# Performance work log

Measured on AMD Instinct MI355X. Metric: run time of the kernel, lower is better.

## Reference

```python
import jax, jax.numpy as jnp
import numpy as np

B, N, F_IN, H = 1, 4096, 256, 4
OUT_F = 256
HEAD_DIM = OUT_F // H
E_RAND = 131072  # avg degree 32
LN_EPS = 1e-5


def setup_inputs() -> dict:
    key = jax.random.key(0)
    ks = jax.random.split(key, 12)
    x = jax.random.normal(ks[0], (B, N, F_IN), jnp.float32)
    # random edges + self-loops so every softmax row has at least one unmasked entry
    src = jax.random.randint(ks[1], (E_RAND,), 0, N, dtype=jnp.int32)
    dst = jax.random.randint(ks[2], (E_RAND,), 0, N, dtype=jnp.int32)
    loops = jnp.arange(N, dtype=jnp.int32)
    edge_index = jnp.stack([jnp.concatenate([loops, src]), jnp.concatenate([loops, dst])])
    s = 1.0 / np.sqrt(F_IN)
    Wq = jax.random.uniform(ks[3], (OUT_F, F_IN), jnp.float32, -s, s)
    bq = jax.random.uniform(ks[4], (OUT_F,), jnp.float32, -s, s)
    Wk = jax.random.uniform(ks[5], (OUT_F, F_IN), jnp.float32, -s, s)
    bk = jax.random.uniform(ks[6], (OUT_F,), jnp.float32, -s, s)
    Wv = jax.random.uniform(ks[7], (OUT_F, F_IN), jnp.float32, -s, s)
    bv = jax.random.uniform(ks[8], (OUT_F,), jnp.float32, -s, s)
    ln_g = jnp.ones((OUT_F,), jnp.float32)
    ln_b = jnp.zeros((OUT_F,), jnp.float32)
    return {"x": x, "edge_index": edge_index, "Wq": Wq, "bq": bq, "Wk": Wk,
            "bk": bk, "Wv": Wv, "bv": bv, "ln_g": ln_g, "ln_b": ln_b}


def _layer_norm(y, g, b):
    mu = jnp.mean(y, axis=-1, keepdims=True)
    var = jnp.mean(jnp.square(y - mu), axis=-1, keepdims=True)
    return (y - mu) * jax.lax.rsqrt(var + LN_EPS) * g + b


def reference(x, edge_index, Wq, bq, Wk, bk, Wv, bv, ln_g, ln_b):
    b, n, f_in = x.shape
    out_f = Wq.shape[0]
    hd = out_f // H
    # linear projections -> [b, H, n, hd]
    Q = (x @ Wq.T + bq).reshape(b, n, H, hd).transpose(0, 2, 1, 3)
    K = (x @ Wk.T + bk).reshape(b, n, H, hd).transpose(0, 2, 1, 3)
    V = (x @ Wv.T + bv).reshape(b, n, H, hd).transpose(0, 2, 1, 3)
    scores = jnp.einsum('bhnd,bhmd->bhnm', Q, K) / jnp.sqrt(jnp.float32(hd))
    # adjacency mask: same for every batch/head (torch scatters identically per b,h)
    adj = jnp.zeros((n, n), bool).at[edge_index[0], edge_index[1]].set(True)
    scores = jnp.where(adj, scores, -jnp.inf)
    attn = jax.nn.softmax(scores, axis=-1)  # dropout = identity (eval)
    out = jnp.einsum('bhnm,bhmd->bhnd', attn, V)
    out = out.transpose(0, 2, 1, 3).reshape(b, n, out_f)
    out = out + x if f_in == out_f else out  # residual
    out = _layer_norm(out, ln_g, ln_b)
    return (out, attn)
```

## Files before the change

kernel.cpp:

```cpp
#include <hip/hip_runtime.h>
#include <stdint.h>

#define NNODES 4096
#define FDIM 256
#define NH 4
#define HD 64
#define MWORDS 128
#define SCAP 512

typedef float f4 __attribute__((ext_vector_type(4)));

__global__ __launch_bounds__(256) void k_transpose_w(
    const float* __restrict__ Wq, const float* __restrict__ Wk,
    const float* __restrict__ Wv, float* __restrict__ Wt)
{
    __shared__ float tile[32][33];
    int mat = blockIdx.z;
    const float* W = mat == 0 ? Wq : (mat == 1 ? Wk : Wv);
    float* dst = Wt + (size_t)mat * FDIM * FDIM;
    int r0 = blockIdx.y * 32, c0 = blockIdx.x * 32;
    int tx = threadIdx.x, ty = threadIdx.y;
    for (int i = ty; i < 32; i += 8)
        tile[i][tx] = W[(size_t)(r0 + i) * FDIM + c0 + tx];
    __syncthreads();
    for (int i = ty; i < 32; i += 8)
        dst[(size_t)(c0 + i) * FDIM + r0 + tx] = tile[tx][i];
}

__global__ void k_mask_build(const int* __restrict__ ei, int E, uint32_t* __restrict__ mask)
{
    int e = blockIdx.x * 256 + threadIdx.x;
    if (e >= E) return;
    int r = ei[e];
    int c = ei[E + e];
    atomicOr(&mask[(size_t)r * MWORDS + (c >> 5)], 1u << (c & 31));
}

#define TN 16
__global__ __launch_bounds__(256) void k_qkv(
    const float* __restrict__ x, const float* __restrict__ Wt,
    const float* __restrict__ bq, const float* __restrict__ bk, const float* __restrict__ bv,
    float* __restrict__ qkv)
{
    int mat = blockIdx.y;
    const float* W = Wt + (size_t)mat * FDIM * FDIM;
    const float* bias = mat == 0 ? bq : (mat == 1 ? bk : bv);
    float* dst = qkv + (size_t)mat * NNODES * FDIM;
    int n0 = blockIdx.x * TN;
    int t = threadIdx.x;
    __shared__ float xl[TN][FDIM + 4];
    for (int f = t; f < TN * (FDIM / 4); f += 256) {
        int n = f >> 6, c4 = f & 63;
        float4 v = ((const float4*)(x + (size_t)(n0 + n) * FDIM))[c4];
        *(float4*)&xl[n][c4 * 4] = v;
    }
    __syncthreads();
    float acc[TN];
    #pragma unroll
    for (int n = 0; n < TN; ++n) acc[n] = 0.f;
    for (int k4 = 0; k4 < FDIM / 4; ++k4) {
        float w0 = W[(size_t)(k4 * 4 + 0) * FDIM + t];
        float w1 = W[(size_t)(k4 * 4 + 1) * FDIM + t];
        float w2 = W[(size_t)(k4 * 4 + 2) * FDIM + t];
        float w3 = W[(size_t)(k4 * 4 + 3) * FDIM + t];
        #pragma unroll
        for (int n = 0; n < TN; ++n) {
            float4 xv = *(const float4*)&xl[n][k4 * 4];
            acc[n] = fmaf(w0, xv.x, acc[n]);
            acc[n] = fmaf(w1, xv.y, acc[n]);
            acc[n] = fmaf(w2, xv.z, acc[n]);
            acc[n] = fmaf(w3, xv.w, acc[n]);
        }
    }
    float bb = bias[t];
    #pragma unroll
    for (int n = 0; n < TN; ++n)
        dst[(size_t)(n0 + n) * FDIM + t] = acc[n] + bb;
}

__global__ __launch_bounds__(256) void k_attn(
    const float* __restrict__ qkv, const uint32_t* __restrict__ mask,
    const float* __restrict__ x, const float* __restrict__ ln_g, const float* __restrict__ ln_b,
    float* __restrict__ out, float* __restrict__ stats)
{
    const float* Q = qkv;
    const float* K = qkv + (size_t)NNODES * FDIM;
    const float* V = qkv + 2 * (size_t)NNODES * FDIM;

    __shared__ float q_lds[FDIM];
    __shared__ uint32_t mrow[MWORDS];
    __shared__ unsigned short list[NNODES];
    __shared__ float sv[NH][SCAP];
    __shared__ float red0[NH], red1[NH];
    __shared__ int cnt_s;

    int n = blockIdx.x;
    int t = threadIdx.x;
    int h = t >> 6, lane = t & 63;

    q_lds[t] = Q[(size_t)n * FDIM + t];
    float xv = x[(size_t)n * FDIM + t];
    if (t < MWORDS) mrow[t] = mask[(size_t)n * MWORDS + t];
    __syncthreads();

    if (t < 64) {
        int total = 0;
        for (int r = 0; r < 2; ++r) {
            int w = r * 64 + t;
            uint32_t bits = mrow[w];
            int c = __popc(bits);
            int scan = c;
            #pragma unroll
            for (int off = 1; off < 64; off <<= 1) {
                int u = __shfl_up(scan, off);
                if (t >= off) scan += u;
            }
            int base = total + scan - c;
            while (bits) {
                int b = __ffs(bits) - 1;
                list[base++] = (unsigned short)(w * 32 + b);
                bits &= bits - 1;
            }
            total += __shfl(scan, 63);
        }
        if (t == 0) cnt_s = total;
    }
    __syncthreads();
    int cnt = cnt_s;

    const float4* qh = (const float4*)(q_lds + h * HD);

    float mi = -INFINITY, li = 0.f;
    for (int i = lane; i < cnt; i += 64) {
        int m = list[i];
        const float4* kp = (const float4*)(K + (size_t)m * FDIM + h * HD);
        float s = 0.f;
        #pragma unroll
        for (int j = 0; j < HD / 4; ++j) {
            float4 a = qh[j], b = kp[j];
            s += a.x * b.x + a.y * b.y + a.z * b.z + a.w * b.w;
        }
        s *= 0.125f;
        if (i < SCAP) sv[h][i] = s;
        float nm = fmaxf(mi, s);
        li = li * __expf(mi - nm) + __expf(s - nm);
        mi = nm;
    }
    #pragma unroll
    for (int off = 32; off; off >>= 1) {
        float mo = __shfl_xor(mi, off);
        float lo = __shfl_xor(li, off);
        float nm = fmaxf(mi, mo);
        float ea = (nm == -INFINITY) ? 0.f : __expf(mi - nm);
        float eb = (nm == -INFINITY) ? 0.f : __expf(mo - nm);
        li = li * ea + lo * eb;
        mi = nm;
    }
    float M = mi;
    float Linv = 1.f / li;
    if (lane == 0) {
        stats[((size_t)h * NNODES + n) * 2 + 0] = M;
        stats[((size_t)h * NNODES + n) * 2 + 1] = Linv;
    }

    int cm = min(cnt, SCAP);
    for (int i = lane; i < cm; i += 64)
        sv[h][i] = __expf(sv[h][i] - M) * Linv;

    const float* vb = V + (size_t)h * HD + lane;
    float o0 = 0.f, o1 = 0.f, o2 = 0.f, o3 = 0.f;
    int j = 0;
    for (; j + 3 < cm; j += 4) {
        int m0 = list[j], m1 = list[j + 1], m2 = list[j + 2], m3 = list[j + 3];
        float p0 = sv[h][j], p1 = sv[h][j + 1], p2 = sv[h][j + 2], p3 = sv[h][j + 3];
        o0 = fmaf(p0, vb[(size_t)m0 * FDIM], o0);
        o1 = fmaf(p1, vb[(size_t)m1 * FDIM], o1);
        o2 = fmaf(p2, vb[(size_t)m2 * FDIM], o2);
        o3 = fmaf(p3, vb[(size_t)m3 * FDIM], o3);
    }
    for (; j < cm; ++j)
        o0 = fmaf(sv[h][j], vb[(size_t)list[j] * FDIM], o0);
    for (; j < cnt; ++j) {
        int m = list[j];
        const float4* kp = (const float4*)(K + (size_t)m * FDIM + h * HD);
        float s = 0.f;
        #pragma unroll
        for (int jj = 0; jj < HD / 4; ++jj) {
            float4 a = qh[jj], b = kp[jj];
            s += a.x * b.x + a.y * b.y + a.z * b.z + a.w * b.w;
        }
        o0 = fmaf(__expf(s * 0.125f - M) * Linv, vb[(size_t)m * FDIM], o0);
    }
    float o = (o0 + o1) + (o2 + o3);

    float y = o + xv;
    float s1 = y, s2 = y * y;
    #pragma unroll
    for (int off = 32; off; off >>= 1) {
        s1 += __shfl_xor(s1, off);
        s2 += __shfl_xor(s2, off);
    }
    if (lane == 0) { red0[h] = s1; red1[h] = s2; }
    __syncthreads();
    float ts1 = (red0[0] + red0[1]) + (red0[2] + red0[3]);
    float ts2 = (red1[0] + red1[1]) + (red1[2] + red1[3]);
    float mu = ts1 * (1.f / 256.f);
    float var = ts2 * (1.f / 256.f) - mu * mu;
    out[(size_t)n * FDIM + t] = (y - mu) * rsqrtf(var + 1e-5f) * ln_g[t] + ln_b[t];
}

__global__ __launch_bounds__(256) void k_scatter(
    const int* __restrict__ ei, int E,
    const float* __restrict__ qkv, const float* __restrict__ stats,
    float* __restrict__ attn)
{
    int idx = blockIdx.x * 256 + threadIdx.x;
    if (idx >= E * NH) return;
    int e = idx >> 2;
    int h = idx & 3;
    int r = ei[e];
    int c = ei[E + e];

    const float* Q = qkv;
    const float* K = qkv + (size_t)NNODES * FDIM;
    const float4* qp = (const float4*)(Q + (size_t)r * FDIM + h * HD);
    const float4* kp = (const float4*)(K + (size_t)c * FDIM + h * HD);
    float s = 0.f;
    #pragma unroll
    for (int j = 0; j < HD / 4; ++j) {
        float4 a = qp[j], b = kp[j];
        s += a.x * b.x + a.y * b.y + a.z * b.z + a.w * b.w;
    }
    size_t row = (size_t)h * NNODES + r;
    float M = stats[row * 2 + 0];
    float Linv = stats[row * 2 + 1];
    attn[row * NNODES + c] = __expf(s * 0.125f - M) * Linv;
}

extern "C" void kernel_launch(void* const* d_in, const int* in_sizes, int n_in,
                              void* d_out, int out_size, void* d_ws, size_t ws_size,
                              hipStream_t stream)
{
    const float* x    = (const float*)d_in[0];
    const int*   ei   = (const int*)d_in[1];
    const float* Wq   = (const float*)d_in[2];
    const float* bq   = (const float*)d_in[3];
    const float* Wk   = (const float*)d_in[4];
    const float* bk   = (const float*)d_in[5];
    const float* Wv   = (const float*)d_in[6];
    const float* bv   = (const float*)d_in[7];
    const float* ln_g = (const float*)d_in[8];
    const float* ln_b = (const float*)d_in[9];
    float* out = (float*)d_out;
    float* attn = out + (size_t)NNODES * FDIM;

    int E = in_sizes[1] / 2;

    float* Wt  = (float*)d_ws;
    float* qkv = Wt + 3 * FDIM * FDIM;
    uint32_t* mask = (uint32_t*)(qkv + 3 * (size_t)NNODES * FDIM);
    float* stats = (float*)(mask + (size_t)NNODES * MWORDS);

    hipMemsetAsync(attn, 0, (size_t)NH * NNODES * NNODES * sizeof(float), stream);
    hipMemsetAsync(mask, 0, (size_t)NNODES * MWORDS * sizeof(uint32_t), stream);

    dim3 tb(32, 8);
    k_transpose_w<<<dim3(8, 8, 3), tb, 0, stream>>>(Wq, Wk, Wv, Wt);
    k_mask_build<<<(E + 255) / 256, 256, 0, stream>>>(ei, E, mask);
    k_qkv<<<dim3(NNODES / TN, 3), 256, 0, stream>>>(x, Wt, bq, bk, bv, qkv);
    k_attn<<<NNODES, 256, 0, stream>>>(qkv, mask, x, ln_g, ln_b, out, stats);
    k_scatter<<<(E * NH + 255) / 256, 256, 0, stream>>>(ei, E, qkv, stats, attn);
}
```

Measured before the change: 221.3 us.

## Split attn zero-fill across compute kernels to overlap memset with work

Removes the monolithic 256MB memset of the attention matrix and instead appends extra fill-only blocks to the qkv, attention and scatter kernels, each zeroing a row range. Scatter is split into two launches so rows are written only after their zero-fill has completed in a prior kernel. The intent is to hide the bandwidth-bound memset behind compute-bound kernels. In exchange it adds an extra scatter launch, and each scatter launch reads and filters every edge.

```diff
diff --git a/kernel.cpp b/kernel.cpp
--- a/kernel.cpp
+++ b/kernel.cpp
@@ -7,8 +7,22 @@
 #define HD 64
 #define MWORDS 128
 #define SCAP 512
+#define TOTROWS (NH * NNODES)
+#define ROW4 (NNODES / 4)
+#define R0 5120
+#define R1 13824
+#define NFB 2048
 
 typedef float f4 __attribute__((ext_vector_type(4)));
+
+__device__ __forceinline__ void fill_zero(f4* __restrict__ attn4, size_t beg, size_t end,
+                                          int fid, int t)
+{
+    f4 z = {0.f, 0.f, 0.f, 0.f};
+    size_t stride = (size_t)NFB * 256;
+    for (size_t i = beg + (size_t)fid * 256 + t; i < end; i += stride)
+        attn4[i] = z;
+}
 
 __global__ __launch_bounds__(256) void k_transpose_w(
     const float* __restrict__ Wq, const float* __restrict__ Wk,
@@ -37,17 +51,21 @@
 }
 
 #define TN 16
-__global__ __launch_bounds__(256) void k_qkv(
+__global__ __launch_bounds__(256) void k_qkv_fill(
     const float* __restrict__ x, const float* __restrict__ Wt,
     const float* __restrict__ bq, const float* __restrict__ bk, const float* __restrict__ bv,
-    float* __restrict__ qkv)
-{
-    int mat = blockIdx.y;
+    float* __restrict__ qkv, float* __restrict__ attn)
+{
+    int t = threadIdx.x;
+    if (blockIdx.x >= 3 * (NNODES / TN)) {
+        fill_zero((f4*)attn, 0, (size_t)R0 * ROW4, blockIdx.x - 3 * (NNODES / TN), t);
+        return;
+    }
+    int mat = blockIdx.x >> 8;
+    int n0 = (blockIdx.x & 255) * TN;
     const float* W = Wt + (size_t)mat * FDIM * FDIM;
     const float* bias = mat == 0 ? bq : (mat == 1 ? bk : bv);
     float* dst = qkv + (size_t)mat * NNODES * FDIM;
-    int n0 = blockIdx.x * TN;
-    int t = threadIdx.x;
     __shared__ float xl[TN][FDIM + 4];
     for (int f = t; f < TN * (FDIM / 4); f += 256) {
         int n = f >> 6, c4 = f & 63;
@@ -78,11 +96,17 @@
         dst[(size_t)(n0 + n) * FDIM + t] = acc[n] + bb;
 }
 
-__global__ __launch_bounds__(256) void k_attn(
+__global__ __launch_bounds__(256) void k_attn_fill(
     const float* __restrict__ qkv, const uint32_t* __restrict__ mask,
     const float* __restrict__ x, const float* __restrict__ ln_g, const float* __restrict__ ln_b,
-    float* __restrict__ out, float* __restrict__ stats)
-{
+    float* __restrict__ out, float* __restrict__ stats, float* __restrict__ attn)
+{
+    int t = threadIdx.x;
+    if (blockIdx.x >= NNODES) {
+        fill_zero((f4*)attn, (size_t)R0 * ROW4, (size_t)R1 * ROW4, blockIdx.x - NNODES, t);
+        return;
+    }
+
     const float* Q = qkv;
     const float* K = qkv + (size_t)NNODES * FDIM;
     const float* V = qkv + 2 * (size_t)NNODES * FDIM;
@@ -95,7 +119,6 @@
     __shared__ int cnt_s;
 
     int n = blockIdx.x;
-    int t = threadIdx.x;
     int h = t >> 6, lane = t & 63;
 
     q_lds[t] = Q[(size_t)n * FDIM + t];
@@ -209,17 +232,25 @@
     out[(size_t)n * FDIM + t] = (y - mu) * rsqrtf(var + 1e-5f) * ln_g[t] + ln_b[t];
 }
 
-__global__ __launch_bounds__(256) void k_scatter(
-    const int* __restrict__ ei, int E,
+__global__ __launch_bounds__(256) void k_scatter_fill(
+    const int* __restrict__ ei, int E, int nsb,
     const float* __restrict__ qkv, const float* __restrict__ stats,
-    float* __restrict__ attn)
-{
-    int idx = blockIdx.x * 256 + threadIdx.x;
+    float* __restrict__ attn, int rowLo, int rowHi,
+    unsigned long long fillBeg, unsigned long long fillEnd)
+{
+    int t = threadIdx.x;
+    if (blockIdx.x >= nsb) {
+        fill_zero((f4*)attn, (size_t)fillBeg, (size_t)fillEnd, blockIdx.x - nsb, t);
+        return;
+    }
+    int idx = blockIdx.x * 256 + t;
     if (idx >= E * NH) return;
     int e = idx >> 2;
     int h = idx & 3;
     int r = ei[e];
     int c = ei[E + e];
+    int row = h * NNODES + r;
+    if (row < rowLo || row >= rowHi) return;
 
     const float* Q = qkv;
     const float* K = qkv + (size_t)NNODES * FDIM;
@@ -231,10 +262,9 @@
         float4 a = qp[j], b = kp[j];
         s += a.x * b.x + a.y * b.y + a.z * b.z + a.w * b.w;
     }
-    size_t row = (size_t)h * NNODES + r;
-    float M = stats[row * 2 + 0];
-    float Linv = stats[row * 2 + 1];
-    attn[row * NNODES + c] = __expf(s * 0.125f - M) * Linv;
+    float M = stats[(size_t)row * 2 + 0];
+    float Linv = stats[(size_t)row * 2 + 1];
+    attn[(size_t)row * NNODES + c] = __expf(s * 0.125f - M) * Linv;
 }
 
 extern "C" void kernel_launch(void* const* d_in, const int* in_sizes, int n_in,
@@ -261,13 +291,21 @@
     uint32_t* mask = (uint32_t*)(qkv + 3 * (size_t)NNODES * FDIM);
     float* stats = (float*)(mask + (size_t)NNODES * MWORDS);
 
-    hipMemsetAsync(attn, 0, (size_t)NH * NNODES * NNODES * sizeof(float), stream);
     hipMemsetAsync(mask, 0, (size_t)NNODES * MWORDS * sizeof(uint32_t), stream);
 
     dim3 tb(32, 8);
     k_transpose_w<<<dim3(8, 8, 3), tb, 0, stream>>>(Wq, Wk, Wv, Wt);
     k_mask_build<<<(E + 255) / 256, 256, 0, stream>>>(ei, E, mask);
-    k_qkv<<<dim3(NNODES / TN, 3), 256, 0, stream>>>(x, Wt, bq, bk, bv, qkv);
-    k_attn<<<NNODES, 256, 0, stream>>>(qkv, mask, x, ln_g, ln_b, out, stats);
-    k_scatter<<<(E * NH + 255) / 256, 256, 0, stream>>>(ei, E, qkv, stats, attn);
-}
+
+    k_qkv_fill<<<3 * (NNODES / TN) + NFB, 256, 0, stream>>>(x, Wt, bq, bk, bv, qkv, attn);
+
+    k_attn_fill<<<NNODES + NFB, 256, 0, stream>>>(qkv, mask, x, ln_g, ln_b, out, stats, attn);
+
+    int nsb = (E * NH + 255) / 256;
+    k_scatter_fill<<<nsb + NFB, 256, 0, stream>>>(
+        ei, E, nsb, qkv, stats, attn, 0, R1,
+        (unsigned long long)R1 * ROW4, (unsigned long long)TOTROWS * ROW4);
+
+    k_scatter_fill<<<nsb, 256, 0, stream>>>(
+        ei, E, nsb, qkv, stats, attn, R1, TOTROWS, 0ull, 0ull);
+}
```

Result: faster. 211.9 us (-4.2%).

## Fuse attention-matrix zero-fill into QKV and attention kernels as extra blocks

Applied to the files above, without the earlier changes.

Removes the separate memset of the 256 MB dense attention output and adds extra zero-fill blocks to the QKV projection and attention kernels. The first 6144 rows are filled alongside QKV and the remaining rows alongside attention. This lets the bandwidth-bound fill overlap with compute-bound work and drops a standalone launch. The costs are larger grids and block-count constants hardcoded to match the fill sizes.

```diff
diff --git a/kernel.cpp b/kernel.cpp
--- a/kernel.cpp
+++ b/kernel.cpp
@@ -7,8 +7,21 @@
 #define HD 64
 #define MWORDS 128
 #define SCAP 512
+#define TOTROWS (NH * NNODES)
+#define ROW4 (NNODES / 4)
+#define R0 6144
+#define FB3 24576
+#define FB4 40960
 
 typedef float f4 __attribute__((ext_vector_type(4)));
+
+__device__ __forceinline__ void fill_one(f4* __restrict__ attn4, size_t beg, size_t end,
+                                         int fid, int t)
+{
+    f4 z = {0.f, 0.f, 0.f, 0.f};
+    size_t i = beg + (size_t)fid * 256 + t;
+    if (i < end) attn4[i] = z;
+}
 
 __global__ __launch_bounds__(256) void k_transpose_w(
     const float* __restrict__ Wq, const float* __restrict__ Wk,
@@ -37,17 +50,21 @@
 }
 
 #define TN 16
-__global__ __launch_bounds__(256) void k_qkv(
+__global__ __launch_bounds__(256) void k_qkv_fill(
     const float* __restrict__ x, const float* __restrict__ Wt,
     const float* __restrict__ bq, const float* __restrict__ bk, const float* __restrict__ bv,
-    float* __restrict__ qkv)
-{
-    int mat = blockIdx.y;
+    float* __restrict__ qkv, float* __restrict__ attn)
+{
+    int t = threadIdx.x;
+    if (blockIdx.x >= 3 * (NNODES / TN)) {
+        fill_one((f4*)attn, 0, (size_t)R0 * ROW4, blockIdx.x - 3 * (NNODES / TN), t);
+        return;
+    }
+    int mat = blockIdx.x >> 8;
+    int n0 = (blockIdx.x & 255) * TN;
     const float* W = Wt + (size_t)mat * FDIM * FDIM;
     const float* bias = mat == 0 ? bq : (mat == 1 ? bk : bv);
     float* dst = qkv + (size_t)mat * NNODES * FDIM;
-    int n0 = blockIdx.x * TN;
-    int t = threadIdx.x;
     __shared__ float xl[TN][FDIM + 4];
     for (int f = t; f < TN * (FDIM / 4); f += 256) {
         int n = f >> 6, c4 = f & 63;
@@ -78,11 +95,17 @@
         dst[(size_t)(n0 + n) * FDIM + t] = acc[n] + bb;
 }
 
-__global__ __launch_bounds__(256) void k_attn(
+__global__ __launch_bounds__(256) void k_attn_fill(
     const float* __restrict__ qkv, const uint32_t* __restrict__ mask,
     const float* __restrict__ x, const float* __restrict__ ln_g, const float* __restrict__ ln_b,
-    float* __restrict__ out, float* __restrict__ stats)
-{
+    float* __restrict__ out, float* __restrict__ stats, float* __restrict__ attn)
+{
+    int t = threadIdx.x;
+    if (blockIdx.x >= NNODES) {
+        fill_one((f4*)attn, (size_t)R0 * ROW4, (size_t)TOTROWS * ROW4, blockIdx.x - NNODES, t);
+        return;
+    }
+
     const float* Q = qkv;
     const float* K = qkv + (size_t)NNODES * FDIM;
     const float* V = qkv + 2 * (size_t)NNODES * FDIM;
@@ -95,7 +118,6 @@
     __shared__ int cnt_s;
 
     int n = blockIdx.x;
-    int t = threadIdx.x;
     int h = t >> 6, lane = t & 63;
 
     q_lds[t] = Q[(size_t)n * FDIM + t];
@@ -261,13 +283,15 @@
     uint32_t* mask = (uint32_t*)(qkv + 3 * (size_t)NNODES * FDIM);
     float* stats = (float*)(mask + (size_t)NNODES * MWORDS);
 
-    hipMemsetAsync(attn, 0, (size_t)NH * NNODES * NNODES * sizeof(float), stream);
     hipMemsetAsync(mask, 0, (size_t)NNODES * MWORDS * sizeof(uint32_t), stream);
 
     dim3 tb(32, 8);
     k_transpose_w<<<dim3(8, 8, 3), tb, 0, stream>>>(Wq, Wk, Wv, Wt);
     k_mask_build<<<(E + 255) / 256, 256, 0, stream>>>(ei, E, mask);
-    k_qkv<<<dim3(NNODES / TN, 3), 256, 0, stream>>>(x, Wt, bq, bk, bv, qkv);
-    k_attn<<<NNODES, 256, 0, stream>>>(qkv, mask, x, ln_g, ln_b, out, stats);
+
+    k_qkv_fill<<<3 * (NNODES / TN) + FB3, 256, 0, stream>>>(x, Wt, bq, bk, bv, qkv, attn);
+
+    k_attn_fill<<<NNODES + FB4, 256, 0, stream>>>(qkv, mask, x, ln_g, ln_b, out, stats, attn);
+
     k_scatter<<<(E * NH + 255) / 256, 256, 0, stream>>>(ei, E, qkv, stats, attn);
 }
```

Result: faster. 206.9 us (-6.5%).
